# Optimization experiments

Measured on AMD Instinct MI355X. Metric: run time of the kernel, lower is better.

## Reference

```python
import jax, jax.numpy as jnp
import numpy as np

NUM_HEADS = 10
LN_EPS = 1e-5

def setup_inputs() -> dict:
    key = jax.random.key(0)
    ks = jax.random.split(key, 8)
    B, H, N, D, Dt = 256, 200, 64, 640, 256
    s = 0.02
    return {
        'clicked_news': jax.random.normal(ks[0], (B, H, D), jnp.float32),
        'clicked_topics': jax.random.normal(ks[1], (B, H, Dt), jnp.float32),
        'cand_topics': jax.random.normal(ks[2], (B, N, Dt), jnp.float32),
        'Wq': jax.random.normal(ks[3], (D, Dt), jnp.float32) * s,
        'bq': jnp.zeros((D,), jnp.float32),
        'Wk': jax.random.normal(ks[4], (D, Dt), jnp.float32) * s,
        'bk': jnp.zeros((D,), jnp.float32),
        'Wv': jax.random.normal(ks[5], (D, D), jnp.float32) * s,
        'bv': jnp.zeros((D,), jnp.float32),
        'Wg': jax.random.normal(ks[6], (D, D), jnp.float32) * s,
        'bg': jnp.zeros((D,), jnp.float32),
        'ln_gamma': jnp.ones((D,), jnp.float32),
        'ln_beta': jnp.zeros((D,), jnp.float32),
    }

def reference(clicked_news, clicked_topics, cand_topics, Wq, bq, Wk, bk, Wv, bv, Wg, bg, ln_gamma, ln_beta):
    B, H, D = clicked_news.shape
    N = cand_topics.shape[1]
    nh = NUM_HEADS
    hd = D // nh
    scale = jnp.sqrt(jnp.asarray(D, clicked_news.dtype))

    Qf = cand_topics @ Wq.T + bq            # [B, N, D]
    Kf = clicked_topics @ Wk.T + bk         # [B, H, D]
    # V projection feeds `weighted`, which is dead code w.r.t. outputs; omitted.

    Q = Qf.reshape(B, N, nh, hd)
    K = Kf.reshape(B, H, nh, hd)
    scores = jnp.einsum('bnhd,bmhd->bhnm', Q, K) / scale   # [B, nh, N, H]
    attn = jax.nn.softmax(scores, axis=-1)                 # dropout is identity in eval

    # query weighting: softmax over candidates of ||Q||
    query_weights = jax.nn.softmax(jnp.linalg.norm(Qf, axis=-1), axis=1)   # [B, N]
    agg = (attn.sum(axis=1) * query_weights[:, :, None]).sum(axis=1)       # [B, H]
    attn_weights_agg = jax.nn.softmax(agg, axis=-1)                        # [B, H]

    weighted_clicked = attn_weights_agg[:, :, None] * clicked_news         # [B, H, D]
    gate = jax.nn.sigmoid(weighted_clicked @ Wg.T + bg)
    out = gate * weighted_clicked + (1.0 - gate) * clicked_news

    mu = out.mean(axis=-1, keepdims=True)
    var = out.var(axis=-1, keepdims=True)
    out = (out - mu) / jnp.sqrt(var + LN_EPS) * ln_gamma + ln_beta
    return out, attn_weights_agg
```

## Files before the change

kernel.cpp:

```cpp
#include <hip/hip_runtime.h>
#include <math.h>

#define B_  256
#define H_  200
#define N_  64
#define D_  640
#define DT_ 256
#define NH_ 10
#define HD_ 64
#define MT_ 13
#define MH_ 25600

typedef __attribute__((ext_vector_type(8))) short bf16x8;
typedef __attribute__((ext_vector_type(4))) float f32x4;

__device__ __forceinline__ float wave_reduce_sum(float v) {
    #pragma unroll
    for (int m = 32; m > 0; m >>= 1) v += __shfl_xor(v, m);
    return v;
}
__device__ __forceinline__ float wave_reduce_max(float v) {
    #pragma unroll
    for (int m = 32; m > 0; m >>= 1) v = fmaxf(v, __shfl_xor(v, m));
    return v;
}
__device__ __forceinline__ float red16_sum(float v) {
    #pragma unroll
    for (int m = 1; m < 16; m <<= 1) v += __shfl_xor(v, m);
    return v;
}
__device__ __forceinline__ float red16_max(float v) {
    #pragma unroll
    for (int m = 1; m < 16; m <<= 1) v = fmaxf(v, __shfl_xor(v, m));
    return v;
}
__device__ __forceinline__ short f2bf(float x) {
    unsigned u = __float_as_uint(x);
    unsigned r = (u + 0x7fffu + ((u >> 16) & 1u)) >> 16;
    return (short)r;
}
__device__ __forceinline__ float bf2f(short s) {
    return __uint_as_float(((unsigned)(unsigned short)s) << 16);
}

__device__ __forceinline__ void gload_lds16(const void* g, void* lds) {
    __builtin_amdgcn_global_load_lds(
        (const __attribute__((address_space(1))) void*)g,
        (__attribute__((address_space(3))) void*)lds, 16, 0, 0);
}

__global__ __launch_bounds__(256) void convert_w(
    const float* __restrict__ src, short* __restrict__ dst, int n)
{
    for (int i = blockIdx.x * 256 + threadIdx.x; i < n; i += gridDim.x * 256)
        dst[i] = f2bf(src[i]);
}

__global__ __launch_bounds__(256, 5) void gemm_bt(
    const float* __restrict__ A, int lda,
    const short* __restrict__ Wb, int ldb,
    const float* __restrict__ bias,
    short* __restrict__ Y, int nkc)
{
    __shared__ float A_f[64 * 64];
    __shared__ short B_lds[128 * 64];
    const int t = threadIdx.x;
    const int lane = t & 63, w = t >> 6;
    const int wm = w >> 1, wn = w & 1;
    const int r16 = lane & 15, g = lane >> 4;
    const int lb = (blockIdx.x & 7) * ((int)gridDim.x >> 3) + (blockIdx.x >> 3);
    const int row0 = (lb / 5) * 64;
    const int col0 = (lb % 5) * 128;

    f32x4 acc[4][2];
    #pragma unroll
    for (int ct = 0; ct < 4; ++ct) {
        acc[ct][0] = (f32x4){0.f,0.f,0.f,0.f};
        acc[ct][1] = (f32x4){0.f,0.f,0.f,0.f};
    }

    for (int k = 0; k < nkc; ++k) {
        const int k0 = k * 64;
        #pragma unroll
        for (int j = 0; j < 4; ++j) {
            const int u = t + j * 256;
            const int row = u >> 4, jj = u & 15;
            gload_lds16(A + (long)(row0 + row) * lda + k0 + ((jj ^ (row & 7)) << 2),
                        (char*)A_f + u * 16);
        }
        #pragma unroll
        for (int j = 0; j < 4; ++j) {
            const int u = t + j * 256;
            const int col = u >> 3, jj = u & 7;
            gload_lds16(Wb + (long)(col0 + col) * ldb + k0 + ((jj ^ (col & 7)) << 3),
                        (char*)B_lds + u * 16);
        }
        __syncthreads();

        #pragma unroll
        for (int kk = 0; kk < 2; ++kk) {
            bf16x8 a[2];
            #pragma unroll
            for (int rt = 0; rt < 2; ++rt) {
                const int row = wm * 32 + rt * 16 + r16;
                const int s = kk * 8 + g * 2;
                float4 f0 = *(const float4*)(A_f + row * 64 + ((s ^ (row & 7)) << 2));
                float4 f1 = *(const float4*)(A_f + row * 64 + (((s + 1) ^ (row & 7)) << 2));
                bf16x8 av;
                av[0] = f2bf(f0.x); av[1] = f2bf(f0.y); av[2] = f2bf(f0.z); av[3] = f2bf(f0.w);
                av[4] = f2bf(f1.x); av[5] = f2bf(f1.y); av[6] = f2bf(f1.z); av[7] = f2bf(f1.w);
                a[rt] = av;
            }
            #pragma unroll
            for (int ct = 0; ct < 4; ++ct) {
                const int col = wn * 64 + ct * 16 + r16;
                const int sb = kk * 4 + g;
                bf16x8 b = *(const bf16x8*)(B_lds + col * 64 + ((sb ^ (col & 7)) << 3));
                acc[ct][0] = __builtin_amdgcn_mfma_f32_16x16x32_bf16(a[0], b, acc[ct][0], 0, 0, 0);
                acc[ct][1] = __builtin_amdgcn_mfma_f32_16x16x32_bf16(a[1], b, acc[ct][1], 0, 0, 0);
            }
        }
        __syncthreads();
    }

    #pragma unroll
    for (int ct = 0; ct < 4; ++ct) {
        const int col = col0 + wn * 64 + ct * 16 + r16;
        const float bv = bias ? bias[col] : 0.f;
        #pragma unroll
        for (int rt = 0; rt < 2; ++rt)
            #pragma unroll
            for (int i = 0; i < 4; ++i)
                Y[(long)(row0 + wm * 32 + rt * 16 + g * 4 + i) * D_ + col] =
                    f2bf(acc[ct][rt][i] + bv);
    }
}

__global__ __launch_bounds__(512, 2) void attn2(
    const short* __restrict__ Qb, const short* __restrict__ Kb,
    float* __restrict__ aw, float* __restrict__ out_tail)
{
    __shared__ short K_l[2][2][208 * 64];
    __shared__ float qn_l[N_];
    __shared__ float qw_l[N_];
    __shared__ float aggp[8][MT_ * 16];
    __shared__ float red2[2];
    const int t = threadIdx.x;
    const int lane = t & 63, w = t >> 6;
    const int wm = w & 3, hh = w >> 2;
    const int r16 = lane & 15, g = lane >> 4;
    const int b = blockIdx.x;
    const int tt = t & 255;
    const int half = t >> 8;

    auto STAGE_K = [&](int bi, int hi) {
        const int h = half * 5 + hi;
        #pragma unroll
        for (int j = 0; j < 7; ++j) {
            const int u = tt + j * 256;
            if (u < 208 * 8) {
                const int row = u >> 3, jg = u & 7;
                gload_lds16(Kb + ((long)(b * H_) + row) * D_ + h * HD_ +
                                ((jg ^ (row & 7)) << 3),
                            (char*)K_l[half][bi] + u * 16);
            }
        }
    };

    STAGE_K(0, 0);

    if (hh == 0) {
        const short* qrow = Qb + ((long)(b * N_ + wm * 16 + r16)) * D_ + g * 160;
        float ss = 0.f;
        #pragma unroll
        for (int j = 0; j < 20; ++j) {
            bf16x8 v = *(const bf16x8*)(qrow + j * 8);
            #pragma unroll
            for (int e = 0; e < 8; ++e) { float f = bf2f(v[e]); ss += f * f; }
        }
        ss += __shfl_xor(ss, 16);
        ss += __shfl_xor(ss, 32);
        if (g == 0) qn_l[wm * 16 + r16] = ss;
    }
    __syncthreads();
    if (w == 0) {
        float v = sqrtf(qn_l[lane]);
        float mx = wave_reduce_max(v);
        float e = __expf(v - mx);
        float s = wave_reduce_sum(e);
        qw_l[lane] = e / s;
    }
    __syncthreads();

    float qwr[4];
    #pragma unroll
    for (int i = 0; i < 4; ++i) qwr[i] = qw_l[wm * 16 + g * 4 + i];

    const float inv_scale = 0.0395284707521047f;
    float aggl[MT_];
    #pragma unroll
    for (int mt = 0; mt < MT_; ++mt) aggl[mt] = 0.f;

    for (int hi = 0; hi < 5; ++hi) {
        const int h = hh * 5 + hi;
        if (hi + 1 < 5) STAGE_K((hi + 1) & 1, hi + 1);

        const short* kl = K_l[hh][hi & 1];
        const short* qbase = Qb + ((long)(b * N_ + wm * 16 + r16)) * D_ + h * HD_ + g * 8;
        bf16x8 a0 = *(const bf16x8*)(qbase);
        bf16x8 a1 = *(const bf16x8*)(qbase + 32);
        bf16x8 kb0[MT_], kb1[MT_];
        #pragma unroll
        for (int mt = 0; mt < MT_; ++mt) {
            const int row = mt * 16 + r16;
            const int s0 = g ^ (row & 7);
            const int s1 = (g + 4) ^ (row & 7);
            kb0[mt] = *(const bf16x8*)(kl + row * 64 + s0 * 8);
            kb1[mt] = *(const bf16x8*)(kl + row * 64 + s1 * 8);
        }
        f32x4 acc[MT_];
        #pragma unroll
        for (int mt = 0; mt < MT_; ++mt) {
            f32x4 z = {0.f,0.f,0.f,0.f};
            z = __builtin_amdgcn_mfma_f32_16x16x32_bf16(a0, kb0[mt], z, 0, 0, 0);
            z = __builtin_amdgcn_mfma_f32_16x16x32_bf16(a1, kb1[mt], z, 0, 0, 0);
            acc[mt] = z;
        }
        const bool tailok = (r16 < 8);
        float mx[4] = {-INFINITY, -INFINITY, -INFINITY, -INFINITY};
        #pragma unroll
        for (int mt = 0; mt < MT_; ++mt) {
            const bool valid = (mt < 12) || tailok;
            #pragma unroll
            for (int i = 0; i < 4; ++i)
                if (valid) mx[i] = fmaxf(mx[i], acc[mt][i]);
        }
        #pragma unroll
        for (int i = 0; i < 4; ++i) mx[i] = red16_max(mx[i]);
        float sum[4] = {0.f, 0.f, 0.f, 0.f};
        #pragma unroll
        for (int mt = 0; mt < MT_; ++mt) {
            const bool valid = (mt < 12) || tailok;
            #pragma unroll
            for (int i = 0; i < 4; ++i) {
                float e = valid ? __expf((acc[mt][i] - mx[i]) * inv_scale) : 0.f;
                acc[mt][i] = e;
                sum[i] += e;
            }
        }
        float fct[4];
        #pragma unroll
        for (int i = 0; i < 4; ++i) fct[i] = qwr[i] / red16_sum(sum[i]);
        #pragma unroll
        for (int mt = 0; mt < MT_; ++mt)
            aggl[mt] += acc[mt][0] * fct[0] + acc[mt][1] * fct[1]
                      + acc[mt][2] * fct[2] + acc[mt][3] * fct[3];

        __syncthreads();
    }

    #pragma unroll
    for (int mt = 0; mt < MT_; ++mt) {
        aggl[mt] += __shfl_xor(aggl[mt], 16);
        aggl[mt] += __shfl_xor(aggl[mt], 32);
    }
    if (g == 0) {
        #pragma unroll
        for (int mt = 0; mt < MT_; ++mt) aggp[w][mt * 16 + r16] = aggl[mt];
    }
    __syncthreads();
    if (t < MT_ * 16) {
        float v = 0.f;
        #pragma unroll
        for (int j = 0; j < 8; ++j) v += aggp[j][t];
        aggp[0][t] = v;
    }
    __syncthreads();
    if (w == 0) {
        float v0 = aggp[0][lane], v1 = aggp[0][lane + 64], v2 = aggp[0][lane + 128];
        const bool has3 = lane < (H_ - 192);
        float v3 = has3 ? aggp[0][lane + 192] : -INFINITY;
        float mx = wave_reduce_max(fmaxf(fmaxf(v0, v1), fmaxf(v2, v3)));
        float s = __expf(v0 - mx) + __expf(v1 - mx) + __expf(v2 - mx)
                + (has3 ? __expf(v3 - mx) : 0.f);
        s = wave_reduce_sum(s);
        if (lane == 0) { red2[0] = mx; red2[1] = s; }
    }
    __syncthreads();
    if (t < H_) {
        float v = __expf(aggp[0][t] - red2[0]) / red2[1];
        aw[b * H_ + t] = v;
        out_tail[b * H_ + t] = v;
    }
}

__global__ __launch_bounds__(256) void blendln(
    const float* __restrict__ cl, const short* __restrict__ Z,
    const float* __restrict__ aw, const float* __restrict__ bg,
    const float* __restrict__ gamma, const float* __restrict__ beta,
    float* __restrict__ out)
{
    const int t = threadIdx.x;
    const int lane = t & 63, w = t >> 6;
    const int row = blockIdx.x * 4 + w;
    const float awr = aw[row];
    const long base = (long)row * D_;

    float o[10];
    float s = 0.f, sq = 0.f;
    #pragma unroll
    for (int i = 0; i < 10; ++i) {
        const int col = lane + 64 * i;
        const float y = bf2f(Z[base + col]);
        const float c = cl[base + col];
        const float z = awr * y + bg[col];
        const float gt = 1.f / (1.f + __expf(-z));
        const float ov = c * (1.f + gt * (awr - 1.f));
        o[i] = ov; s += ov; sq += ov * ov;
    }
    s  = wave_reduce_sum(s);
    sq = wave_reduce_sum(sq);
    const float mu  = s * (1.f / D_);
    const float var = sq * (1.f / D_) - mu * mu;
    const float ri  = 1.0f / sqrtf(var + 1e-5f);
    #pragma unroll
    for (int i = 0; i < 10; ++i) {
        const int col = lane + 64 * i;
        out[base + col] = (o[i] - mu) * ri * gamma[col] + beta[col];
    }
}

extern "C" void kernel_launch(void* const* d_in, const int* in_sizes, int n_in,
                              void* d_out, int out_size, void* d_ws, size_t ws_size,
                              hipStream_t stream) {
    const float* clicked_news   = (const float*)d_in[0];
    const float* clicked_topics = (const float*)d_in[1];
    const float* cand_topics    = (const float*)d_in[2];
    const float* Wq = (const float*)d_in[3];
    const float* bq = (const float*)d_in[4];
    const float* Wk = (const float*)d_in[5];
    const float* bk = (const float*)d_in[6];
    const float* Wg = (const float*)d_in[9];
    const float* bg = (const float*)d_in[10];
    const float* ln_gamma = (const float*)d_in[11];
    const float* ln_beta  = (const float*)d_in[12];

    float* out = (float*)d_out;
    float* ws  = (float*)d_ws;

    float* aw   = ws;
    short* Wq_b = (short*)(aw + (long)B_ * H_);
    short* Wk_b = Wq_b + (long)D_ * DT_;
    short* Wg_b = Wk_b + (long)D_ * DT_;
    short* Qb   = Wg_b + (long)D_ * D_;
    short* Z    = Qb;
    short* Kb = (short*)d_out;
    float* out_tail = out + (long)B_ * H_ * D_;

    convert_w<<<128, 256, 0, stream>>>(Wq, Wq_b, D_ * DT_);
    convert_w<<<128, 256, 0, stream>>>(Wk, Wk_b, D_ * DT_);
    convert_w<<<256, 256, 0, stream>>>(Wg, Wg_b, D_ * D_);

    gemm_bt<<<1280, 256, 0, stream>>>(cand_topics, DT_, Wq_b, DT_, bq, Qb, 4);
    gemm_bt<<<4000, 256, 0, stream>>>(clicked_topics, DT_, Wk_b, DT_, bk, Kb, 4);
    attn2<<<B_, 512, 0, stream>>>(Qb, Kb, aw, out_tail);

    for (int h = 0; h < 2; ++h) {
        const long off = (long)h * MH_;
        gemm_bt<<<2000, 256, 0, stream>>>(clicked_news + off * D_, D_,
                                          Wg_b, D_, nullptr, Z, 10);
        blendln<<<MH_ / 4, 256, 0, stream>>>(
            clicked_news + off * D_, Z, aw + off, bg, ln_gamma, ln_beta,
            out + off * D_);
    }
}
```

Baseline: 273.9 us.

## Fuse gate blend into Wg GEMM epilogue and merge weight conversions

The gate sigmoid and blend move into the epilogue of the Wg GEMM, which writes the blended value as bf16 along with per-row partial sums and sums of squares. A lightweight LN kernel then reduces those partials and normalizes. The bf16 Z is still written and read, but the second kernel no longer re-reads the fp32 clicked_news. The three weight-conversion launches become one. The cost is a strided, less coalesced epilogue read of A, bf16 rounding of the pre-LN values, and an extra partials buffer in the workspace.

```diff
diff --git a/kernel.cpp b/kernel.cpp
--- a/kernel.cpp
+++ b/kernel.cpp
@@ -49,11 +49,17 @@
         (__attribute__((address_space(3))) void*)lds, 16, 0, 0);
 }
 
-__global__ __launch_bounds__(256) void convert_w(
-    const float* __restrict__ src, short* __restrict__ dst, int n)
+__global__ __launch_bounds__(256) void convert3(
+    const float* __restrict__ s0, short* __restrict__ d0, int n0,
+    const float* __restrict__ s1, short* __restrict__ d1, int n1,
+    const float* __restrict__ s2, short* __restrict__ d2, int n2)
 {
-    for (int i = blockIdx.x * 256 + threadIdx.x; i < n; i += gridDim.x * 256)
-        dst[i] = f2bf(src[i]);
+    const int total = n0 + n1 + n2;
+    for (int i = blockIdx.x * 256 + threadIdx.x; i < total; i += gridDim.x * 256) {
+        if (i < n0)            d0[i] = f2bf(s0[i]);
+        else if (i < n0 + n1)  d1[i - n0] = f2bf(s1[i - n0]);
+        else                   d2[i - n0 - n1] = f2bf(s2[i - n0 - n1]);
+    }
 }
 
 __global__ __launch_bounds__(256, 5) void gemm_bt(
@@ -133,6 +139,152 @@
             for (int i = 0; i < 4; ++i)
                 Y[(long)(row0 + wm * 32 + rt * 16 + g * 4 + i) * D_ + col] =
                     f2bf(acc[ct][rt][i] + bv);
+    }
+}
+
+__global__ __launch_bounds__(256, 5) void gemm_gate(
+    const float* __restrict__ A,
+    const short* __restrict__ Wb,
+    const float* __restrict__ aw,
+    const float* __restrict__ bg,
+    short* __restrict__ Z,
+    float* __restrict__ part)
+{
+    __shared__ float A_f[64 * 64];
+    __shared__ short B_lds[128 * 64];
+    const int t = threadIdx.x;
+    const int lane = t & 63, w = t >> 6;
+    const int wm = w >> 1, wn = w & 1;
+    const int r16 = lane & 15, g = lane >> 4;
+    const int lb = (blockIdx.x & 7) * ((int)gridDim.x >> 3) + (blockIdx.x >> 3);
+    const int row0 = (lb / 5) * 64;
+    const int col0 = (lb % 5) * 128;
+    const int strip = col0 >> 7;
+
+    f32x4 acc[4][2];
+    #pragma unroll
+    for (int ct = 0; ct < 4; ++ct) {
+        acc[ct][0] = (f32x4){0.f,0.f,0.f,0.f};
+        acc[ct][1] = (f32x4){0.f,0.f,0.f,0.f};
+    }
+
+    for (int k = 0; k < 10; ++k) {
+        const int k0 = k * 64;
+        #pragma unroll
+        for (int j = 0; j < 4; ++j) {
+            const int u = t + j * 256;
+            const int row = u >> 4, jj = u & 15;
+            gload_lds16(A + (long)(row0 + row) * D_ + k0 + ((jj ^ (row & 7)) << 2),
+                        (char*)A_f + u * 16);
+        }
+        #pragma unroll
+        for (int j = 0; j < 4; ++j) {
+            const int u = t + j * 256;
+            const int col = u >> 3, jj = u & 7;
+            gload_lds16(Wb + (long)(col0 + col) * D_ + k0 + ((jj ^ (col & 7)) << 3),
+                        (char*)B_lds + u * 16);
+        }
+        __syncthreads();
+
+        #pragma unroll
+        for (int kk = 0; kk < 2; ++kk) {
+            bf16x8 a[2];
+            #pragma unroll
+            for (int rt = 0; rt < 2; ++rt) {
+                const int row = wm * 32 + rt * 16 + r16;
+                const int s = kk * 8 + g * 2;
+                float4 f0 = *(const float4*)(A_f + row * 64 + ((s ^ (row & 7)) << 2));
+                float4 f1 = *(const float4*)(A_f + row * 64 + (((s + 1) ^ (row & 7)) << 2));
+                bf16x8 av;
+                av[0] = f2bf(f0.x); av[1] = f2bf(f0.y); av[2] = f2bf(f0.z); av[3] = f2bf(f0.w);
+                av[4] = f2bf(f1.x); av[5] = f2bf(f1.y); av[6] = f2bf(f1.z); av[7] = f2bf(f1.w);
+                a[rt] = av;
+            }
+            #pragma unroll
+            for (int ct = 0; ct < 4; ++ct) {
+                const int col = wn * 64 + ct * 16 + r16;
+                const int sb = kk * 4 + g;
+                bf16x8 b = *(const bf16x8*)(B_lds + col * 64 + ((sb ^ (col & 7)) << 3));
+                acc[ct][0] = __builtin_amdgcn_mfma_f32_16x16x32_bf16(a[0], b, acc[ct][0], 0, 0, 0);
+                acc[ct][1] = __builtin_amdgcn_mfma_f32_16x16x32_bf16(a[1], b, acc[ct][1], 0, 0, 0);
+            }
+        }
+        __syncthreads();
+    }
+
+    float awv[2][4];
+    #pragma unroll
+    for (int rt = 0; rt < 2; ++rt)
+        #pragma unroll
+        for (int i = 0; i < 4; ++i)
+            awv[rt][i] = aw[row0 + wm * 32 + rt * 16 + g * 4 + i];
+
+    float ps[2][4], pq[2][4];
+    #pragma unroll
+    for (int rt = 0; rt < 2; ++rt)
+        #pragma unroll
+        for (int i = 0; i < 4; ++i) { ps[rt][i] = 0.f; pq[rt][i] = 0.f; }
+
+    #pragma unroll
+    for (int ct = 0; ct < 4; ++ct) {
+        const int col = col0 + wn * 64 + ct * 16 + r16;
+        const float bgv = bg[col];
+        #pragma unroll
+        for (int rt = 0; rt < 2; ++rt)
+            #pragma unroll
+            for (int i = 0; i < 4; ++i) {
+                const int row = row0 + wm * 32 + rt * 16 + g * 4 + i;
+                const float awr = awv[rt][i];
+                const float cl = A[(long)row * D_ + col];
+                const float z  = awr * acc[ct][rt][i] + bgv;
+                const float gt = 1.f / (1.f + __expf(-z));
+                const float o  = cl * (1.f + gt * (awr - 1.f));
+                const short ob = f2bf(o);
+                const float of = bf2f(ob);
+                Z[(long)row * D_ + col] = ob;
+                ps[rt][i] += of; pq[rt][i] += of * of;
+            }
+    }
+    #pragma unroll
+    for (int rt = 0; rt < 2; ++rt)
+        #pragma unroll
+        for (int i = 0; i < 4; ++i) {
+            const float s = red16_sum(ps[rt][i]);
+            const float q = red16_sum(pq[rt][i]);
+            if (r16 == 0) {
+                const int row = row0 + wm * 32 + rt * 16 + g * 4 + i;
+                const long idx = ((long)row * 10 + strip * 2 + wn) * 2;
+                part[idx]     = s;
+                part[idx + 1] = q;
+            }
+        }
+}
+
+__global__ __launch_bounds__(256) void ln_final(
+    const short* __restrict__ Z, const float* __restrict__ part,
+    const float* __restrict__ gamma, const float* __restrict__ beta,
+    float* __restrict__ out)
+{
+    const int t = threadIdx.x;
+    const int lane = t & 63, w = t >> 6;
+    const int row = blockIdx.x * 4 + w;
+    const long base = (long)row * D_;
+
+    float s = 0.f, q = 0.f;
+    #pragma unroll
+    for (int j = 0; j < 10; ++j) {
+        s += part[((long)row * 10 + j) * 2];
+        q += part[((long)row * 10 + j) * 2 + 1];
+    }
+    const float mu  = s * (1.f / D_);
+    const float var = q * (1.f / D_) - mu * mu;
+    const float ri  = 1.0f / sqrtf(var + 1e-5f);
+
+    #pragma unroll
+    for (int i = 0; i < 10; ++i) {
+        const int col = lane + 64 * i;
+        const float o = bf2f(Z[base + col]);
+        out[base + col] = (o - mu) * ri * gamma[col] + beta[col];
     }
 }
 
@@ -294,42 +446,6 @@
     }
 }
 
-__global__ __launch_bounds__(256) void blendln(
-    const float* __restrict__ cl, const short* __restrict__ Z,
-    const float* __restrict__ aw, const float* __restrict__ bg,
-    const float* __restrict__ gamma, const float* __restrict__ beta,
-    float* __restrict__ out)
-{
-    const int t = threadIdx.x;
-    const int lane = t & 63, w = t >> 6;
-    const int row = blockIdx.x * 4 + w;
-    const float awr = aw[row];
-    const long base = (long)row * D_;
-
-    float o[10];
-    float s = 0.f, sq = 0.f;
-    #pragma unroll
-    for (int i = 0; i < 10; ++i) {
-        const int col = lane + 64 * i;
-        const float y = bf2f(Z[base + col]);
-        const float c = cl[base + col];
-        const float z = awr * y + bg[col];
-        const float gt = 1.f / (1.f + __expf(-z));
-        const float ov = c * (1.f + gt * (awr - 1.f));
-        o[i] = ov; s += ov; sq += ov * ov;
-    }
-    s  = wave_reduce_sum(s);
-    sq = wave_reduce_sum(sq);
-    const float mu  = s * (1.f / D_);
-    const float var = sq * (1.f / D_) - mu * mu;
-    const float ri  = 1.0f / sqrtf(var + 1e-5f);
-    #pragma unroll
-    for (int i = 0; i < 10; ++i) {
-        const int col = lane + 64 * i;
-        out[base + col] = (o[i] - mu) * ri * gamma[col] + beta[col];
-    }
-}
-
 extern "C" void kernel_launch(void* const* d_in, const int* in_sizes, int n_in,
                               void* d_out, int out_size, void* d_ws, size_t ws_size,
                               hipStream_t stream) {
@@ -354,12 +470,13 @@
     short* Wg_b = Wk_b + (long)D_ * DT_;
     short* Qb   = Wg_b + (long)D_ * D_;
     short* Z    = Qb;
+    float* part = (float*)(Z + (long)MH_ * D_);
     short* Kb = (short*)d_out;
     float* out_tail = out + (long)B_ * H_ * D_;
 
-    convert_w<<<128, 256, 0, stream>>>(Wq, Wq_b, D_ * DT_);
-    convert_w<<<128, 256, 0, stream>>>(Wk, Wk_b, D_ * DT_);
-    convert_w<<<256, 256, 0, stream>>>(Wg, Wg_b, D_ * D_);
+    convert3<<<1440, 256, 0, stream>>>(Wq, Wq_b, D_ * DT_,
+                                       Wk, Wk_b, D_ * DT_,
+                                       Wg, Wg_b, D_ * D_);
 
     gemm_bt<<<1280, 256, 0, stream>>>(cand_topics, DT_, Wq_b, DT_, bq, Qb, 4);
     gemm_bt<<<4000, 256, 0, stream>>>(clicked_topics, DT_, Wk_b, DT_, bk, Kb, 4);
@@ -367,10 +484,9 @@
 
     for (int h = 0; h < 2; ++h) {
         const long off = (long)h * MH_;
-        gemm_bt<<<2000, 256, 0, stream>>>(clicked_news + off * D_, D_,
-                                          Wg_b, D_, nullptr, Z, 10);
-        blendln<<<MH_ / 4, 256, 0, stream>>>(
-            clicked_news + off * D_, Z, aw + off, bg, ln_gamma, ln_beta,
-            out + off * D_);
-    }
-}
+        gemm_gate<<<2000, 256, 0, stream>>>(clicked_news + off * D_, Wg_b,
+                                            aw + off, bg, Z, part);
+        ln_final<<<MH_ / 4, 256, 0, stream>>>(Z, part, ln_gamma, ln_beta,
+                                              out + off * D_);
+    }
+}
```

Result: slower. 283.2 us (+3.4%).
